# Kernel tuning notes

Hardware: AMD Instinct MI355X
Metric: run time of the kernel (lower is better)

## Reference

```python
import jax, jax.numpy as jnp
import numpy as np

NUM_CURVE_BINS = 32
NUM_HIST_BINS = 64
W_L1, W_FF, W_LAB, W_MS, W_CURVE, W_HIST, W_WIN = 1.0, 0.3, 0.4, 0.3, 0.4, 0.2, 0.5


def _rgb_to_lab(rgb):
    # rgb: [B,3,H,W] in [0,1]
    M = jnp.array([[0.4124564, 0.3575761, 0.1804375],
                   [0.2126729, 0.7151522, 0.0721750],
                   [0.0193339, 0.1191920, 0.9503041]], dtype=rgb.dtype)
    white = jnp.array([0.95047, 1.0, 1.08883], dtype=rgb.dtype)
    lin = jnp.where(rgb > 0.04045, ((rgb + 0.055) / 1.055) ** 2.4, rgb / 12.92)
    xyz = jnp.einsum('bchw,xc->bxhw', lin, M) / white[None, :, None, None]
    delta = 6.0 / 29.0
    cond = xyz > delta ** 3
    # safe cube root to avoid nan grads at 0 in the unused branch
    f = jnp.where(cond, jnp.maximum(xyz, delta ** 3) ** (1.0 / 3.0),
                  xyz / (3 * delta ** 2) + 4.0 / 29.0)
    L = 116.0 * f[:, 1:2] - 16.0
    a = 500.0 * (f[:, 0:1] - f[:, 1:2])
    b = 200.0 * (f[:, 1:2] - f[:, 2:3])
    return jnp.concatenate([L, a, b], axis=1)


def _avg_pool2(x):
    B, C, H, W = x.shape
    return x.reshape(B, C, H // 2, 2, W // 2, 2).mean(axis=(3, 5))


def _avg_pool11(x):
    # avg_pool2d k=11, stride=1, pad=5, count_include_pad=True
    s = jax.lax.reduce_window(x, 0.0, jax.lax.add, (1, 1, 11, 11), (1, 1, 1, 1),
                              [(0, 0), (0, 0), (5, 5), (5, 5)])
    return s / 121.0


def _soft_hist_cum(x):
    B, C, H, W = x.shape
    centers = jnp.linspace(0.0, 1.0, NUM_HIST_BINS).astype(x.dtype)
    bw = 1.0 / NUM_HIST_BINS
    xf = x.reshape(B, C, H * W, 1)
    w = jnp.exp(-(xf - centers) ** 2 / (2.0 * bw * bw))  # [B,C,HW,bins]
    h = w.sum(axis=2)
    h = h / (h.sum(axis=-1, keepdims=True) + 1e-7)
    return jnp.cumsum(h, axis=-1)


def _hsv_sv(rgb):
    mx = rgb.max(axis=1, keepdims=True)
    mn = rgb.min(axis=1, keepdims=True)
    diff = mx - mn + 1e-7
    return diff / (mx + 1e-7), mx  # (s, v)


def _forward(pred, target, input_img):
    # --- L1 ---
    l1 = jnp.mean(jnp.abs(pred - target))
    # --- Focal frequency (alpha=1, loss_weight=1) ---
    pf = jnp.abs(jnp.fft.rfft2(pred, norm='ortho'))
    tf = jnp.abs(jnp.fft.rfft2(target, norm='ortho'))
    d = jnp.abs(tf - pf)
    w = d / (jnp.mean(d) + 1e-8)
    ff = jnp.mean(w * d)
    # --- LAB perceptual (l_weight=1, ab_weight=2) ---
    pl = _rgb_to_lab(pred)
    tl = _rgb_to_lab(target)
    l_loss = jnp.mean(jnp.abs(pl[:, 0:1] - tl[:, 0:1])) / 100.0
    ab_loss = jnp.mean(jnp.abs(pl[:, 1:3] - tl[:, 1:3])) / 128.0
    lab = 1.0 * l_loss + 2.0 * ab_loss
    # --- Multi-scale ---
    ph, th = _avg_pool2(pred), _avg_pool2(target)
    pq, tq = _avg_pool2(ph), _avg_pool2(th)
    ms = (l1 + jnp.mean(jnp.abs(ph - th)) + jnp.mean(jnp.abs(pq - tq))) / 3.0
    # --- Color curve: per-channel binned means over input_img bins ---
    idx = jnp.clip((input_img * NUM_CURVE_BINS).astype(jnp.int32), 0, NUM_CURVE_BINS - 1)
    seg = (idx + NUM_CURVE_BINS * jnp.arange(3, dtype=jnp.int32)[None, :, None, None]).reshape(-1)
    ns = 3 * NUM_CURVE_BINS
    cnt = jax.ops.segment_sum(jnp.ones(seg.shape, dtype=pred.dtype), seg, num_segments=ns)
    ps = jax.ops.segment_sum(pred.reshape(-1), seg, num_segments=ns)
    ts = jax.ops.segment_sum(target.reshape(-1), seg, num_segments=ns)
    safe_cnt = jnp.maximum(cnt, 1.0)
    pc = jnp.where(cnt > 0, ps / safe_cnt, 0.0)
    tc = jnp.where(cnt > 0, ts / safe_cnt, 0.0)
    curve = jnp.mean(jnp.abs(pc - tc))  # == avg over 3 channels of per-channel bin-mean L1
    # --- Histogram matching (cumulative, EMD approx) ---
    hl = jnp.mean(jnp.abs(_soft_hist_cum(pred) - _soft_hist_cum(target)))
    # --- Window boost ---
    t_s, t_v = _hsv_sv(target)
    mask = ((t_v > 0.6) & (t_s > 0.2)).astype(pred.dtype)
    mask = _avg_pool11(mask)
    wloss = (jnp.abs(pred - target) * mask).sum() / (mask.sum() * 3.0 + 1e-7)
    p_s, _ = _hsv_sv(pred)
    sat = (jnp.abs(p_s - t_s) * mask).sum() / (mask.sum() + 1e-7)
    wb = wloss + 0.5 * sat
    total = (W_L1 * l1 + W_FF * ff + W_LAB * lab + W_MS * ms
             + W_CURVE * curve + W_HIST * hl + W_WIN * wb)
    return total


def setup_inputs() -> dict:
    key = jax.random.key(0)
    k1, k2, k3 = jax.random.split(key, 3)
    shp = (8, 3, 256, 256)
    return {
        'pred': jax.random.uniform(k1, shp, dtype=jnp.float32),
        'target': jax.random.uniform(k2, shp, dtype=jnp.float32),
        'input_img': jax.random.uniform(k3, shp, dtype=jnp.float32),
    }


def reference(pred, target, input_img):
    return _forward(pred, target, input_img)
```

## Files before the change

kernel.cpp:

```cpp
#include <hip/hip_runtime.h>
#include <math.h>

#define HW 65536
#define NPX 524288
#define NEL 1572864

#define P_POINT 4096
#define P_MS    10240
#define P_WIN   11008
#define P_FFT   12544
#define P_CURVE 13360
#define P_HIST  31792
#define MASK_OFF 65536
#define FFT_P   589824
#define FFT_T   (FFT_P + 24*66048)

#define CURVE_SCALE 131072.0f

#define B_POINT 2048
#define B_MS    384
#define B_CURVE 192
#define B_HIST  384
#define B_FFTR  1536
#define G_MEGA1 (B_POINT+B_MS+B_CURVE+B_HIST+B_FFTR)
#define B_WIN   512
#define B_FFTC  408
#define G_MEGA2 (B_WIN+B_FFTC)

__device__ __forceinline__ float fpow24(float x) {
    return __builtin_amdgcn_exp2f(2.4f * __builtin_amdgcn_logf(x));
}
__device__ __forceinline__ float fcbrt(float x) {
    return __builtin_amdgcn_exp2f((1.0f/3.0f) * __builtin_amdgcn_logf(x));
}
__device__ __forceinline__ float labF(float t) {
    return t > 0.008856452f ? fcbrt(t) : t * 7.787037f + 0.13793103f;
}
__device__ __forceinline__ void rgb2lab(float r, float g, float b,
                                        float& L, float& A, float& Bc) {
    float lr = r > 0.04045f ? fpow24((r + 0.055f) * (1.0f/1.055f)) : r * (1.0f/12.92f);
    float lg = g > 0.04045f ? fpow24((g + 0.055f) * (1.0f/1.055f)) : g * (1.0f/12.92f);
    float lb = b > 0.04045f ? fpow24((b + 0.055f) * (1.0f/1.055f)) : b * (1.0f/12.92f);
    float X = (0.4124564f*lr + 0.3575761f*lg + 0.1804375f*lb) * (1.0f/0.95047f);
    float Y = (0.2126729f*lr + 0.7151522f*lg + 0.0721750f*lb);
    float Z = (0.0193339f*lr + 0.1191920f*lg + 0.9503041f*lb) * (1.0f/1.08883f);
    float fx = labF(X), fy = labF(Y), fz = labF(Z);
    L = 116.f*fy - 16.f;
    A = 500.f*(fx - fy);
    Bc = 200.f*(fy - fz);
}

__device__ __forceinline__ float blockSum(float v, float* sb) {
    #pragma unroll
    for (int o = 32; o > 0; o >>= 1) v += __shfl_down(v, o, 64);
    int lane = threadIdx.x & 63, w = threadIdx.x >> 6;
    if (lane == 0) sb[w] = v;
    __syncthreads();
    float r = 0.f;
    if (threadIdx.x == 0) {
        int nw = (blockDim.x + 63) >> 6;
        for (int i = 0; i < nw; ++i) r += sb[i];
    }
    __syncthreads();
    return r;
}

__global__ __launch_bounds__(256) void k_mega1(const float* __restrict__ pred,
                                               const float* __restrict__ targ,
                                               const float* __restrict__ inp,
                                               float* __restrict__ ws) {
    __shared__ __align__(16) unsigned char sm[17408];
    int tid = threadIdx.x;
    int bid = blockIdx.x;

    if (bid < B_POINT) {
        float* sb = (float*)sm;
        int i = bid*256 + tid;
        int b = i >> 16, hw = i & 65535;
        const float* p = pred + b*3*HW + hw;
        const float* t = targ + b*3*HW + hw;
        float pr = p[0], pg = p[HW], pb = p[2*HW];
        float tr = t[0], tg = t[HW], tb = t[2*HW];
        float e3 = fabsf(pr-tr) + fabsf(pg-tg) + fabsf(pb-tb);
        float Lp,Ap,Bp, Lt,At,Bt;
        rgb2lab(pr,pg,pb, Lp,Ap,Bp);
        rgb2lab(tr,tg,tb, Lt,At,Bt);
        float sL = fabsf(Lp-Lt);
        float sab = fabsf(Ap-At) + fabsf(Bp-Bt);
        float tmx = fmaxf(tr, fmaxf(tg, tb)), tmn = fminf(tr, fminf(tg, tb));
        float tsat = (tmx - tmn + 1e-7f) / (tmx + 1e-7f);
        ws[MASK_OFF + i] = (tmx > 0.6f && tsat > 0.2f) ? 1.f : 0.f;
        float v;
        v = blockSum(e3, sb);  if (tid == 0) ws[P_POINT + bid] = v;
        v = blockSum(sL, sb);  if (tid == 0) ws[P_POINT + 2048 + bid] = v;
        v = blockSum(sab, sb); if (tid == 0) ws[P_POINT + 4096 + bid] = v;
    } else if (bid < B_POINT + B_MS) {
        float* sb = (float*)sm;
        int blk = bid - B_POINT;
        int t = blk*256 + tid;
        int sc = t >> 12;
        int q = t & 4095;
        int y4 = q >> 6, x4 = q & 63;
        const float* pp = pred + sc*HW + (y4*4)*256 + x4*4;
        const float* tp = targ + sc*HW + (y4*4)*256 + x4*4;
        float4 p0 = *(const float4*)(pp);
        float4 p1 = *(const float4*)(pp + 256);
        float4 p2 = *(const float4*)(pp + 512);
        float4 p3 = *(const float4*)(pp + 768);
        float4 q0 = *(const float4*)(tp);
        float4 q1 = *(const float4*)(tp + 256);
        float4 q2 = *(const float4*)(tp + 512);
        float4 q3 = *(const float4*)(tp + 768);
        float a00 = (p0.x+p0.y+p1.x+p1.y)*0.25f, a01 = (p0.z+p0.w+p1.z+p1.w)*0.25f;
        float a10 = (p2.x+p2.y+p3.x+p3.y)*0.25f, a11 = (p2.z+p2.w+p3.z+p3.w)*0.25f;
        float b00 = (q0.x+q0.y+q1.x+q1.y)*0.25f, b01 = (q0.z+q0.w+q1.z+q1.w)*0.25f;
        float b10 = (q2.x+q2.y+q3.x+q3.y)*0.25f, b11 = (q2.z+q2.w+q3.z+q3.w)*0.25f;
        float s2 = fabsf(a00-b00)+fabsf(a01-b01)+fabsf(a10-b10)+fabsf(a11-b11);
        float s4 = fabsf((a00+a01+a10+a11)*0.25f - (b00+b01+b10+b11)*0.25f);
        float v;
        v = blockSum(s2, sb); if (tid == 0) ws[P_MS + blk] = v;
        v = blockSum(s4, sb); if (tid == 0) ws[P_MS + 384 + blk] = v;
    } else if (bid < B_POINT + B_MS + B_CURVE) {
        unsigned* h = (unsigned*)sm;
        if (tid < 256) h[tid] = 0u;
        if (tid < 32) h[256 + tid] = 0u;
        __syncthreads();
        int blk = bid - (B_POINT + B_MS);
        int slice = blk >> 3, part = blk & 7;
        int c = slice % 3;
        int base = slice * HW + part * 8192;
        const float4* ip = (const float4*)(inp + base);
        const float4* pp = (const float4*)(pred + base);
        const float4* tp = (const float4*)(targ + base);
        int segbase = 32 * c;
        #pragma unroll
        for (int it = 0; it < 8; ++it) {
            float4 a = ip[it*256 + tid];
            float4 p = pp[it*256 + tid];
            float4 t = tp[it*256 + tid];
            float av[4] = {a.x, a.y, a.z, a.w};
            float pv[4] = {p.x, p.y, p.z, p.w};
            float tv[4] = {t.x, t.y, t.z, t.w};
            #pragma unroll
            for (int j = 0; j < 4; ++j) {
                int idx = (int)(av[j] * 32.f);
                idx = min(max(idx, 0), 31);
                unsigned s3 = (unsigned)((segbase + idx) * 3);
                atomicAdd(&h[s3],     1u);
                atomicAdd(&h[s3 + 1], (unsigned)__float2uint_rn(pv[j] * CURVE_SCALE));
                atomicAdd(&h[s3 + 2], (unsigned)__float2uint_rn(tv[j] * CURVE_SCALE));
            }
        }
        __syncthreads();
        if (tid < 96) {
            unsigned v = h[segbase*3 + tid];
            int q = tid - (tid/3)*3;
            float f = (q == 0) ? (float)v : (float)v * (1.f/CURVE_SCALE);
            ws[P_CURVE + blk*96 + tid] = f;
        }
    } else if (bid < B_POINT + B_MS + B_CURVE + B_HIST) {
        unsigned (*fh)[1024] = (unsigned(*)[1024])sm;
        float* wtab = (float*)(sm + 16384);
        int hb = bid - (B_POINT + B_MS + B_CURVE);
        int s = hb >> 3, part = hb & 7;
        const float* src = (s < 24 ? pred + s*HW : targ + (s-24)*HW) + part*8192;
        #pragma unroll
        for (int j = 0; j < 16; ++j) ((unsigned*)sm)[tid + 256*j] = 0u;
        if (tid < 193) {
            float d = (float)(tid - 96);
            wtab[tid] = __builtin_amdgcn_exp2f(-0.002907957f * d * d);
        }
        __syncthreads();
        int wv = tid >> 6;
        const float4* s4 = (const float4*)src;
        #pragma unroll
        for (int it = 0; it < 8; ++it) {
            float4 v = s4[it*256 + tid];
            float vals[4] = {v.x, v.y, v.z, v.w};
            #pragma unroll
            for (int e = 0; e < 4; ++e) {
                unsigned f = __float2uint_rn(vals[e] * 1008.f);
                f = min(f, 1008u);
                atomicAdd(&fh[wv][f], 1u);
            }
        }
        __syncthreads();
        #pragma unroll
        for (int j = 0; j < 4; ++j) {
            int idx = tid + 256*j;
            fh[0][idx] = fh[0][idx] + fh[1][idx] + fh[2][idx] + fh[3][idx];
        }
        __syncthreads();
        int k = tid >> 2, q = tid & 3;
        float acc = 0.f;
        for (int i = q; i < 193; i += 4) {
            int f = 16*k + i - 96;
            if (f >= 0 && f <= 1008) acc += (float)fh[0][f] * wtab[i];
        }
        acc += __shfl_xor(acc, 1, 64);
        acc += __shfl_xor(acc, 2, 64);
        if (q == 0) ws[P_HIST + hb*64 + k] = acc;
    } else {
        float (*re4)[256] = (float(*)[256])sm;
        float (*im4)[256] = (float(*)[256])(sm + 4096);
        int fb = bid - (B_POINT + B_MS + B_CURVE + B_HIST);
        int fid = tid >> 6, l = tid & 63;
        int g = fb*4 + fid;
        int s = g >> 7, pr = g & 127;
        const float* src = (s < 24 ? pred + s*HW : targ + (s-24)*HW) + (2*pr)*256;
        float* re = re4[fid];
        float* im = im4[fid];
        #pragma unroll
        for (int j = 0; j < 4; ++j) {
            int x = l + 64*j;
            re[x] = src[x];
            im[x] = src[256 + x];
        }
        __syncthreads();
        #pragma unroll
        for (int st = 0; st < 8; ++st) {
            int m = 256 >> st, half = m >> 1, sh = 7 - st;
            #pragma unroll
            for (int kk = 0; kk < 2; ++kk) {
                int bb = l + 64*kk;
                int j = bb & (half - 1);
                int i0 = ((bb >> sh) << (sh + 1)) + j;
                int i1 = i0 + half;
                float ang = -6.283185307f * (float)j / (float)m;
                float si, co;
                __sincosf(ang, &si, &co);
                float ur = re[i0], ui = im[i0];
                float vr = re[i1], vi = im[i1];
                re[i0] = ur + vr;
                im[i0] = ui + vi;
                float dr = ur - vr, di = ui - vi;
                re[i1] = dr*co - di*si;
                im[i1] = dr*si + di*co;
            }
            __syncthreads();
        }
        float2* outbase = (float2*)(ws + (s < 24 ? FFT_P + s*66048 : FFT_T + (s-24)*66048));
        float2* outA = outbase + (2*pr)*129;
        float2* outB = outbase + (2*pr+1)*129;
        #pragma unroll
        for (int kk = 0; kk < 2; ++kk) {
            int k = l + 64*kk;
            int kb  = __brev((unsigned)k) >> 24;
            int kmb = __brev((unsigned)((256 - k) & 255)) >> 24;
            float zr = re[kb], zi = im[kb];
            float wr = re[kmb], wi = im[kmb];
            outA[k] = make_float2(0.5f*(zr + wr), 0.5f*(zi - wi));
            outB[k] = make_float2(0.5f*(zi + wi), 0.5f*(wr - zr));
        }
        if (l == 0) {
            int kb = __brev(128u) >> 24;
            float zr = re[kb], zi = im[kb];
            outA[128] = make_float2(zr, 0.f);
            outB[128] = make_float2(zi, 0.f);
        }
    }
}

__global__ __launch_bounds__(256) void k_mega2(const float* __restrict__ pred,
                                               const float* __restrict__ targ,
                                               float* __restrict__ ws) {
    __shared__ __align__(16) unsigned char sm[34880];
    int tid = threadIdx.x;
    int bid = blockIdx.x;

    if (bid < B_WIN) {
        float (*msk)[256] = (float(*)[256])sm;
        float (*hs)[256]  = (float(*)[256])(sm + 14336);
        float* sb = (float*)(sm + 28672);
        int b = bid >> 6, strip = bid & 63;
        int y0 = strip * 4;
        int x = tid;
        const float* mbase = ws + MASK_OFF + b*HW;
        #pragma unroll
        for (int r = 0; r < 14; ++r) {
            int yy = y0 - 5 + r;
            msk[r][x] = (yy >= 0 && yy < 256) ? mbase[yy*256 + x] : 0.f;
        }
        __syncthreads();
        #pragma unroll
        for (int r = 0; r < 14; ++r) {
            float hsum = 0.f;
            #pragma unroll
            for (int dx = -5; dx <= 5; ++dx) {
                int xx = x + dx;
                if (xx >= 0 && xx < 256) hsum += msk[r][xx];
            }
            hs[r][x] = hsum;
        }
        __syncthreads();
        float acc_e3 = 0.f, acc_sd = 0.f, acc_m = 0.f;
        #pragma unroll
        for (int j = 0; j < 4; ++j) {
            int ry = y0 + j;
            float vs = 0.f;
            #pragma unroll
            for (int dy = 0; dy < 11; ++dy) vs += hs[j + dy][x];
            float m = vs * (1.f/121.f);
            const float* p = pred + b*3*HW + ry*256 + x;
            const float* t = targ + b*3*HW + ry*256 + x;
            float pr = p[0], pg = p[HW], pb = p[2*HW];
            float tr = t[0], tg = t[HW], tb = t[2*HW];
            float e3 = fabsf(pr-tr) + fabsf(pg-tg) + fabsf(pb-tb);
            float tmx = fmaxf(tr, fmaxf(tg, tb)), tmn = fminf(tr, fminf(tg, tb));
            float tsat = (tmx - tmn + 1e-7f) / (tmx + 1e-7f);
            float pmx = fmaxf(pr, fmaxf(pg, pb)), pmn = fminf(pr, fminf(pg, pb));
            float psat = (pmx - pmn + 1e-7f) / (pmx + 1e-7f);
            acc_e3 += e3 * m;
            acc_sd += fabsf(psat - tsat) * m;
            acc_m  += m;
        }
        float v;
        v = blockSum(acc_e3, sb); if (tid == 0) ws[P_WIN + bid] = v;
        v = blockSum(acc_sd, sb); if (tid == 0) ws[P_WIN + 512 + bid] = v;
        v = blockSum(acc_m,  sb); if (tid == 0) ws[P_WIN + 1024 + bid] = v;
    } else {
        float (*re_)[272] = (float(*)[272])sm;
        float (*im_)[272] = (float(*)[272])(sm + 17408);
        float* sb = (float*)(sm + 34816);
        int cb = bid - B_WIN;
        int s = cb / 17, kt = cb - s*17;
        int k0 = kt * 8;
        const float2* srcP = (const float2*)(ws + FFT_P) + s*33024;
        const float2* srcT = (const float2*)(ws + FFT_T) + s*33024;
        int kk = tid & 7, r0 = tid >> 3;
        int col = k0 + kk;
        bool valid = (col <= 128);
        #pragma unroll
        for (int rb = 0; rb < 8; ++rb) {
            int r = r0 + rb*32;
            float2 vp = valid ? srcP[r*129 + col] : make_float2(0.f, 0.f);
            re_[kk][r] = vp.x; im_[kk][r] = vp.y;
            float2 vt = valid ? srcT[r*129 + col] : make_float2(0.f, 0.f);
            re_[8 + kk][r] = vt.x; im_[8 + kk][r] = vt.y;
        }
        __syncthreads();
        int fid = tid >> 4, w = tid & 15;
        float* re = re_[fid];
        float* im = im_[fid];
        #pragma unroll
        for (int st = 0; st < 8; ++st) {
            int m = 256 >> st, half = m >> 1, sh = 7 - st;
            #pragma unroll
            for (int q = 0; q < 8; ++q) {
                int bb = w + (q << 4);
                int j = bb & (half - 1);
                int i0 = ((bb >> sh) << (sh + 1)) + j;
                int i1 = i0 + half;
                float ang = -6.283185307f * (float)j / (float)m;
                float si, co;
                __sincosf(ang, &si, &co);
                float ur = re[i0], ui = im[i0];
                float vr = re[i1], vi = im[i1];
                re[i0] = ur + vr;
                im[i0] = ui + vi;
                float dr = ur - vr, di = ui - vi;
                re[i1] = dr*co - di*si;
                im[i1] = dr*si + di*co;
            }
            __syncthreads();
        }
        float d1 = 0.f, d2 = 0.f;
        #pragma unroll
        for (int e = 0; e < 8; ++e) {
            int idx = tid + e*256;
            int k = idx >> 8, r = idx & 255;
            if (k0 + k <= 128) {
                float pr2 = re_[k][r]*re_[k][r] + im_[k][r]*im_[k][r];
                float tr2 = re_[8+k][r]*re_[8+k][r] + im_[8+k][r]*im_[8+k][r];
                float d = fabsf(sqrtf(tr2) - sqrtf(pr2)) * (1.f/256.f);
                d1 += d; d2 += d*d;
            }
        }
        float v;
        v = blockSum(d1, sb); if (tid == 0) ws[P_FFT + cb] = v;
        v = blockSum(d2, sb); if (tid == 0) ws[P_FFT + 408 + cb] = v;
    }
}

__global__ __launch_bounds__(256) void k_final(const float* __restrict__ ws,
                                               float* __restrict__ out) {
    __shared__ float shist[3072];
    __shared__ float scn[288];
    __shared__ float red[256];
    __shared__ float sb[8];
    int tid = threadIdx.x;
    for (int q = tid; q < 3072; q += 256) {
        int s = q >> 6, k = q & 63;
        float t = 0.f;
        const float* base = ws + P_HIST + s*8*64 + k;
        #pragma unroll
        for (int p = 0; p < 8; ++p) t += base[p*64];
        shist[q] = t;
    }
    for (int pj = tid; pj < 288; pj += 256) {
        int c = pj / 96, j = pj - c*96;
        float acc = 0.f;
        #pragma unroll
        for (int t = 0; t < 8; ++t) {
            const float* base = ws + P_CURVE + (8*c + 24*t)*96 + j;
            #pragma unroll
            for (int p = 0; p < 8; ++p) acc += base[p*96];
        }
        scn[pj] = acc;
    }
    float a0=0.f, a1=0.f, a2=0.f;
    for (int i = tid; i < 2048; i += 256) {
        a0 += ws[P_POINT + i];
        a1 += ws[P_POINT + 2048 + i];
        a2 += ws[P_POINT + 4096 + i];
    }
    float w0=0.f, w1=0.f, w2=0.f;
    for (int i = tid; i < 512; i += 256) {
        w0 += ws[P_WIN + i];
        w1 += ws[P_WIN + 512 + i];
        w2 += ws[P_WIN + 1024 + i];
    }
    float m0=0.f, m1=0.f;
    for (int i = tid; i < 384; i += 256) {
        m0 += ws[P_MS + i];
        m1 += ws[P_MS + 384 + i];
    }
    float f0=0.f, f1=0.f;
    for (int i = tid; i < 408; i += 256) {
        f0 += ws[P_FFT + i];
        f1 += ws[P_FFT + 408 + i];
    }
    float sum_e3 = blockSum(a0, sb);
    float sum_L  = blockSum(a1, sb);
    float sum_ab = blockSum(a2, sb);
    float wnum   = blockSum(w0, sb);
    float wsat   = blockSum(w1, sb);
    float wm     = blockSum(w2, sb);
    float S2     = blockSum(m0, sb);
    float S4     = blockSum(m1, sb);
    float d1     = blockSum(f0, sb);
    float d2     = blockSum(f1, sb);
    __syncthreads();
    float cv = 0.f;
    if (tid < 96) {
        int c = tid >> 5, i = tid & 31;
        float cnt = scn[c*96 + 3*i];
        float ps  = scn[c*96 + 3*i + 1];
        float ts  = scn[c*96 + 3*i + 2];
        if (cnt > 0.f) cv = fabsf(ps - ts) / cnt;
    }
    red[tid] = cv;
    __syncthreads();
    for (int o = 128; o > 0; o >>= 1) { if (tid < o) red[tid] += red[tid + o]; __syncthreads(); }
    float curve = red[0] / 96.f;
    __syncthreads();
    float hacc = 0.f;
    if (tid < 24) {
        const float* hp = shist + tid*64;
        const float* ht = shist + (24 + tid)*64;
        float sp = 0.f, stt = 0.f;
        for (int k = 0; k < 64; ++k) { sp += hp[k]; stt += ht[k]; }
        float ip = 1.f / (sp + 1e-7f), it = 1.f / (stt + 1e-7f);
        float cp = 0.f, ct = 0.f;
        for (int k = 0; k < 64; ++k) {
            cp += hp[k] * ip;
            ct += ht[k] * it;
            hacc += fabsf(cp - ct);
        }
    }
    red[tid] = hacc;
    __syncthreads();
    for (int o = 128; o > 0; o >>= 1) { if (tid < o) red[tid] += red[tid + o]; __syncthreads(); }
    float hl = red[0] / 1536.f;
    if (tid == 0) {
        float l1  = sum_e3 / (float)NEL;
        float lab = (sum_L / (float)NPX) * 0.01f + 2.f * (sum_ab / (2.f * (float)NPX * 128.f));
        float ms  = (l1 + S2 / 393216.f + S4 / 98304.f) * (1.f/3.f);
        const float M = 792576.f;
        float ff  = (d2 / M) / (d1 / M + 1e-8f);
        float wb  = wnum / (wm*3.f + 1e-7f) + 0.5f * (wsat / (wm + 1e-7f));
        out[0] = l1 + 0.3f*ff + 0.4f*lab + 0.3f*ms + 0.4f*curve + 0.2f*hl + 0.5f*wb;
    }
}

extern "C" void kernel_launch(void* const* d_in, const int* in_sizes, int n_in,
                              void* d_out, int out_size, void* d_ws, size_t ws_size,
                              hipStream_t stream) {
    const float* pred = (const float*)d_in[0];
    const float* targ = (const float*)d_in[1];
    const float* inp  = (const float*)d_in[2];
    float* ws = (float*)d_ws;
    float* out = (float*)d_out;

    k_mega1<<<G_MEGA1, 256, 0, stream>>>(pred, targ, inp, ws);
    k_mega2<<<G_MEGA2, 256, 0, stream>>>(pred, targ, ws);
    k_final<<<1,       256, 0, stream>>>(ws, out);
}
```

Measured before the change: 61.63 us.

## Move window-boost pass into first kernel, recomputing mask from target directly

The window-mask blocks move from the second kernel into the first mega-kernel. They now compute the saturation/value mask on the fly from target pixels instead of reading a mask buffer that the point blocks wrote to the workspace, and the 11x11 box filter now does the vertical sum before the horizontal one. This removes the mask store and reload and leaves the second kernel with only the column FFT blocks. The trade-offs are redundant target reads across each 14-row halo and more shared memory per block in the first kernel, which may lower its occupancy.

```diff
diff --git a/kernel.cpp b/kernel.cpp
--- a/kernel.cpp
+++ b/kernel.cpp
@@ -11,8 +11,7 @@
 #define P_FFT   12544
 #define P_CURVE 13360
 #define P_HIST  31792
-#define MASK_OFF 65536
-#define FFT_P   589824
+#define FFT_P   65536
 #define FFT_T   (FFT_P + 24*66048)
 
 #define CURVE_SCALE 131072.0f
@@ -22,10 +21,9 @@
 #define B_CURVE 192
 #define B_HIST  384
 #define B_FFTR  1536
-#define G_MEGA1 (B_POINT+B_MS+B_CURVE+B_HIST+B_FFTR)
 #define B_WIN   512
-#define B_FFTC  408
-#define G_MEGA2 (B_WIN+B_FFTC)
+#define G_MEGA1 (B_POINT+B_MS+B_CURVE+B_HIST+B_FFTR+B_WIN)
+#define G_MEGA2 408
 
 __device__ __forceinline__ float fpow24(float x) {
     return __builtin_amdgcn_exp2f(2.4f * __builtin_amdgcn_logf(x));
@@ -49,6 +47,11 @@
     A = 500.f*(fx - fy);
     Bc = 200.f*(fy - fz);
 }
+__device__ __forceinline__ float maskOf(float tr, float tg, float tb) {
+    float tmx = fmaxf(tr, fmaxf(tg, tb)), tmn = fminf(tr, fminf(tg, tb));
+    float tsat = (tmx - tmn + 1e-7f) / (tmx + 1e-7f);
+    return (tmx > 0.6f && tsat > 0.2f) ? 1.f : 0.f;
+}
 
 __device__ __forceinline__ float blockSum(float v, float* sb) {
     #pragma unroll
@@ -69,7 +72,7 @@
                                                const float* __restrict__ targ,
                                                const float* __restrict__ inp,
                                                float* __restrict__ ws) {
-    __shared__ __align__(16) unsigned char sm[17408];
+    __shared__ __align__(16) unsigned char sm[18560];
     int tid = threadIdx.x;
     int bid = blockIdx.x;
 
@@ -87,9 +90,6 @@
         rgb2lab(tr,tg,tb, Lt,At,Bt);
         float sL = fabsf(Lp-Lt);
         float sab = fabsf(Ap-At) + fabsf(Bp-Bt);
-        float tmx = fmaxf(tr, fmaxf(tg, tb)), tmn = fminf(tr, fminf(tg, tb));
-        float tsat = (tmx - tmn + 1e-7f) / (tmx + 1e-7f);
-        ws[MASK_OFF + i] = (tmx > 0.6f && tsat > 0.2f) ? 1.f : 0.f;
         float v;
         v = blockSum(e3, sb);  if (tid == 0) ws[P_POINT + bid] = v;
         v = blockSum(sL, sb);  if (tid == 0) ws[P_POINT + 2048 + bid] = v;
@@ -200,7 +200,7 @@
         acc += __shfl_xor(acc, 1, 64);
         acc += __shfl_xor(acc, 2, 64);
         if (q == 0) ws[P_HIST + hb*64 + k] = acc;
-    } else {
+    } else if (bid < B_POINT + B_MS + B_CURVE + B_HIST + B_FFTR) {
         float (*re4)[256] = (float(*)[256])sm;
         float (*im4)[256] = (float(*)[256])(sm + 4096);
         int fb = bid - (B_POINT + B_MS + B_CURVE + B_HIST);
@@ -258,49 +258,45 @@
             outA[128] = make_float2(zr, 0.f);
             outB[128] = make_float2(zi, 0.f);
         }
-    }
-}
-
-__global__ __launch_bounds__(256) void k_mega2(const float* __restrict__ pred,
-                                               const float* __restrict__ targ,
-                                               float* __restrict__ ws) {
-    __shared__ __align__(16) unsigned char sm[34880];
-    int tid = threadIdx.x;
-    int bid = blockIdx.x;
-
-    if (bid < B_WIN) {
+    } else {
         float (*msk)[256] = (float(*)[256])sm;
-        float (*hs)[256]  = (float(*)[256])(sm + 14336);
-        float* sb = (float*)(sm + 28672);
-        int b = bid >> 6, strip = bid & 63;
+        float (*vs)[256]  = (float(*)[256])(sm + 14336);
+        float* sb = (float*)(sm + 18432);
+        int wb = bid - (B_POINT + B_MS + B_CURVE + B_HIST + B_FFTR);
+        int b = wb >> 6, strip = wb & 63;
         int y0 = strip * 4;
         int x = tid;
-        const float* mbase = ws + MASK_OFF + b*HW;
+        const float* tb_ = targ + b*3*HW;
         #pragma unroll
         for (int r = 0; r < 14; ++r) {
             int yy = y0 - 5 + r;
-            msk[r][x] = (yy >= 0 && yy < 256) ? mbase[yy*256 + x] : 0.f;
-        }
-        __syncthreads();
-        #pragma unroll
-        for (int r = 0; r < 14; ++r) {
+            float mv = 0.f;
+            if (yy >= 0 && yy < 256) {
+                int off = yy*256 + x;
+                mv = maskOf(tb_[off], tb_[HW + off], tb_[2*HW + off]);
+            }
+            msk[r][x] = mv;
+        }
+        __syncthreads();
+        #pragma unroll
+        for (int j = 0; j < 4; ++j) {
+            float v = 0.f;
+            #pragma unroll
+            for (int dy = 0; dy < 11; ++dy) v += msk[j + dy][x];
+            vs[j][x] = v;
+        }
+        __syncthreads();
+        float acc_e3 = 0.f, acc_sd = 0.f, acc_m = 0.f;
+        #pragma unroll
+        for (int j = 0; j < 4; ++j) {
+            int ry = y0 + j;
             float hsum = 0.f;
             #pragma unroll
             for (int dx = -5; dx <= 5; ++dx) {
                 int xx = x + dx;
-                if (xx >= 0 && xx < 256) hsum += msk[r][xx];
+                if (xx >= 0 && xx < 256) hsum += vs[j][xx];
             }
-            hs[r][x] = hsum;
-        }
-        __syncthreads();
-        float acc_e3 = 0.f, acc_sd = 0.f, acc_m = 0.f;
-        #pragma unroll
-        for (int j = 0; j < 4; ++j) {
-            int ry = y0 + j;
-            float vs = 0.f;
-            #pragma unroll
-            for (int dy = 0; dy < 11; ++dy) vs += hs[j + dy][x];
-            float m = vs * (1.f/121.f);
+            float m = hsum * (1.f/121.f);
             const float* p = pred + b*3*HW + ry*256 + x;
             const float* t = targ + b*3*HW + ry*256 + x;
             float pr = p[0], pg = p[HW], pb = p[2*HW];
@@ -315,71 +311,75 @@
             acc_m  += m;
         }
         float v;
-        v = blockSum(acc_e3, sb); if (tid == 0) ws[P_WIN + bid] = v;
-        v = blockSum(acc_sd, sb); if (tid == 0) ws[P_WIN + 512 + bid] = v;
-        v = blockSum(acc_m,  sb); if (tid == 0) ws[P_WIN + 1024 + bid] = v;
-    } else {
-        float (*re_)[272] = (float(*)[272])sm;
-        float (*im_)[272] = (float(*)[272])(sm + 17408);
-        float* sb = (float*)(sm + 34816);
-        int cb = bid - B_WIN;
-        int s = cb / 17, kt = cb - s*17;
-        int k0 = kt * 8;
-        const float2* srcP = (const float2*)(ws + FFT_P) + s*33024;
-        const float2* srcT = (const float2*)(ws + FFT_T) + s*33024;
-        int kk = tid & 7, r0 = tid >> 3;
-        int col = k0 + kk;
-        bool valid = (col <= 128);
-        #pragma unroll
-        for (int rb = 0; rb < 8; ++rb) {
-            int r = r0 + rb*32;
-            float2 vp = valid ? srcP[r*129 + col] : make_float2(0.f, 0.f);
-            re_[kk][r] = vp.x; im_[kk][r] = vp.y;
-            float2 vt = valid ? srcT[r*129 + col] : make_float2(0.f, 0.f);
-            re_[8 + kk][r] = vt.x; im_[8 + kk][r] = vt.y;
-        }
-        __syncthreads();
-        int fid = tid >> 4, w = tid & 15;
-        float* re = re_[fid];
-        float* im = im_[fid];
-        #pragma unroll
-        for (int st = 0; st < 8; ++st) {
-            int m = 256 >> st, half = m >> 1, sh = 7 - st;
-            #pragma unroll
-            for (int q = 0; q < 8; ++q) {
-                int bb = w + (q << 4);
-                int j = bb & (half - 1);
-                int i0 = ((bb >> sh) << (sh + 1)) + j;
-                int i1 = i0 + half;
-                float ang = -6.283185307f * (float)j / (float)m;
-                float si, co;
-                __sincosf(ang, &si, &co);
-                float ur = re[i0], ui = im[i0];
-                float vr = re[i1], vi = im[i1];
-                re[i0] = ur + vr;
-                im[i0] = ui + vi;
-                float dr = ur - vr, di = ui - vi;
-                re[i1] = dr*co - di*si;
-                im[i1] = dr*si + di*co;
-            }
-            __syncthreads();
-        }
-        float d1 = 0.f, d2 = 0.f;
-        #pragma unroll
-        for (int e = 0; e < 8; ++e) {
-            int idx = tid + e*256;
-            int k = idx >> 8, r = idx & 255;
-            if (k0 + k <= 128) {
-                float pr2 = re_[k][r]*re_[k][r] + im_[k][r]*im_[k][r];
-                float tr2 = re_[8+k][r]*re_[8+k][r] + im_[8+k][r]*im_[8+k][r];
-                float d = fabsf(sqrtf(tr2) - sqrtf(pr2)) * (1.f/256.f);
-                d1 += d; d2 += d*d;
-            }
-        }
-        float v;
-        v = blockSum(d1, sb); if (tid == 0) ws[P_FFT + cb] = v;
-        v = blockSum(d2, sb); if (tid == 0) ws[P_FFT + 408 + cb] = v;
-    }
+        v = blockSum(acc_e3, sb); if (tid == 0) ws[P_WIN + wb] = v;
+        v = blockSum(acc_sd, sb); if (tid == 0) ws[P_WIN + 512 + wb] = v;
+        v = blockSum(acc_m,  sb); if (tid == 0) ws[P_WIN + 1024 + wb] = v;
+    }
+}
+
+__global__ __launch_bounds__(256) void k_mega2(float* __restrict__ ws) {
+    __shared__ __align__(16) unsigned char sm[34880];
+    int tid = threadIdx.x;
+    int cb = blockIdx.x;
+    float (*re_)[272] = (float(*)[272])sm;
+    float (*im_)[272] = (float(*)[272])(sm + 17408);
+    float* sb = (float*)(sm + 34816);
+    int s = cb / 17, kt = cb - s*17;
+    int k0 = kt * 8;
+    const float2* srcP = (const float2*)(ws + FFT_P) + s*33024;
+    const float2* srcT = (const float2*)(ws + FFT_T) + s*33024;
+    int kk = tid & 7, r0 = tid >> 3;
+    int col = k0 + kk;
+    bool valid = (col <= 128);
+    #pragma unroll
+    for (int rb = 0; rb < 8; ++rb) {
+        int r = r0 + rb*32;
+        float2 vp = valid ? srcP[r*129 + col] : make_float2(0.f, 0.f);
+        re_[kk][r] = vp.x; im_[kk][r] = vp.y;
+        float2 vt = valid ? srcT[r*129 + col] : make_float2(0.f, 0.f);
+        re_[8 + kk][r] = vt.x; im_[8 + kk][r] = vt.y;
+    }
+    __syncthreads();
+    int fid = tid >> 4, w = tid & 15;
+    float* re = re_[fid];
+    float* im = im_[fid];
+    #pragma unroll
+    for (int st = 0; st < 8; ++st) {
+        int m = 256 >> st, half = m >> 1, sh = 7 - st;
+        #pragma unroll
+        for (int q = 0; q < 8; ++q) {
+            int bb = w + (q << 4);
+            int j = bb & (half - 1);
+            int i0 = ((bb >> sh) << (sh + 1)) + j;
+            int i1 = i0 + half;
+            float ang = -6.283185307f * (float)j / (float)m;
+            float si, co;
+            __sincosf(ang, &si, &co);
+            float ur = re[i0], ui = im[i0];
+            float vr = re[i1], vi = im[i1];
+            re[i0] = ur + vr;
+            im[i0] = ui + vi;
+            float dr = ur - vr, di = ui - vi;
+            re[i1] = dr*co - di*si;
+            im[i1] = dr*si + di*co;
+        }
+        __syncthreads();
+    }
+    float d1 = 0.f, d2 = 0.f;
+    #pragma unroll
+    for (int e = 0; e < 8; ++e) {
+        int idx = tid + e*256;
+        int k = idx >> 8, r = idx & 255;
+        if (k0 + k <= 128) {
+            float pr2 = re_[k][r]*re_[k][r] + im_[k][r]*im_[k][r];
+            float tr2 = re_[8+k][r]*re_[8+k][r] + im_[8+k][r]*im_[8+k][r];
+            float d = fabsf(sqrtf(tr2) - sqrtf(pr2)) * (1.f/256.f);
+            d1 += d; d2 += d*d;
+        }
+    }
+    float v;
+    v = blockSum(d1, sb); if (tid == 0) ws[P_FFT + cb] = v;
+    v = blockSum(d2, sb); if (tid == 0) ws[P_FFT + 408 + cb] = v;
 }
 
 __global__ __launch_bounds__(256) void k_final(const float* __restrict__ ws,
@@ -493,6 +493,6 @@
     float* out = (float*)d_out;
 
     k_mega1<<<G_MEGA1, 256, 0, stream>>>(pred, targ, inp, ws);
-    k_mega2<<<G_MEGA2, 256, 0, stream>>>(pred, targ, ws);
+    k_mega2<<<G_MEGA2, 256, 0, stream>>>(ws);
     k_final<<<1,       256, 0, stream>>>(ws, out);
 }
```

Result: slower. 64.53 us (+4.7%).
